# Optimization experiments

Hardware: AMD Instinct MI355X
Metric: run time of the kernel (lower is better)

Reference implementation:

```python
import jax, jax.numpy as jnp
import numpy as np

N = 100000
E = 1600000
IN_FEATS = 128
OUT_FEATS = 32


def setup_inputs() -> dict:
    key = jax.random.key(0)
    k1, k2, k3, k4, k5, k6 = jax.random.split(key, 6)
    features = jax.random.normal(k1, (N, IN_FEATS), dtype=jnp.float32)
    src = jax.random.randint(k2, (E,), 0, N, dtype=jnp.int32)
    dst = jax.random.randint(k3, (E,), 0, N, dtype=jnp.int32)
    # xavier_normal-like scale for fc_weight, attn vectors
    gain = float(np.sqrt(2.0))  # calculate_gain('relu')
    fc_std = gain * np.sqrt(2.0 / (IN_FEATS + OUT_FEATS))
    at_std = gain * np.sqrt(2.0 / (1 + OUT_FEATS))
    fc_weight = jax.random.normal(k4, (IN_FEATS, OUT_FEATS), dtype=jnp.float32) * fc_std
    attn_l = jax.random.normal(k5, (OUT_FEATS,), dtype=jnp.float32) * at_std
    attn_r = jax.random.normal(k6, (OUT_FEATS,), dtype=jnp.float32) * at_std
    return {"features": features, "src": src, "dst": dst,
            "fc_weight": fc_weight, "attn_l": attn_l, "attn_r": attn_r}


def reference(features, src, dst, fc_weight, attn_l, attn_r):
    # dense projection: [N, out]
    h = features @ fc_weight
    # per-node attention logits (GSDDMM operands)
    el = (h * attn_l).sum(-1)  # [N]
    er = (h * attn_r).sum(-1)  # [N]
    # SDDMM: edge score = el[u] + er[v], LeakyReLU(0.2)
    e = jax.nn.leaky_relu(el[src] + er[dst], negative_slope=0.2)  # [E]
    # edge softmax over destination node
    m = jax.ops.segment_max(e, dst, num_segments=N)  # [N], -inf for isolated nodes
    m = jnp.where(jnp.isfinite(m), m, 0.0)
    ex = jnp.exp(e - m[dst])
    s = jax.ops.segment_sum(ex, dst, num_segments=N)  # [N]
    alpha = ex / s[dst]  # [E]
    # SpMM: out[v] = sum_{(u,v) in E} h[u] * alpha[(u,v)]
    out = jax.ops.segment_sum(h[src] * alpha[:, None], dst, num_segments=N)  # [N, out]
    return out
```

## Files before the change

kernel.cpp:

```cpp
#include <hip/hip_runtime.h>
#include <math.h>

#define IN_FEATS 128
#define OUT_FEATS 32
#define BSHIFT 8
#define NPB 256
#define KMAX 512
#define CHUNK 4096
#define PEPT 8
#define CAPL 5120
#define RPT 5

__device__ __forceinline__ unsigned short f2bf(float f) {
    unsigned int u = __float_as_uint(f);
    u += 0x7FFFu + ((u >> 16) & 1u);
    return (unsigned short)(u >> 16);
}
__device__ __forceinline__ float bf2f_lo(unsigned int v) {
    return __uint_as_float(v << 16);
}
__device__ __forceinline__ float bf2f_hi(unsigned int v) {
    return __uint_as_float(v & 0xFFFF0000u);
}

__global__ __launch_bounds__(256) void proj_kernel(
    const float* __restrict__ features,
    const float* __restrict__ W,
    const float* __restrict__ attn_l,
    const float* __restrict__ attn_r,
    unsigned short* __restrict__ h,
    float* __restrict__ el,
    float* __restrict__ er,
    int N)
{
    __shared__ float Ws[IN_FEATS * OUT_FEATS];
    __shared__ float featT[4][IN_FEATS][16];

    const int t  = threadIdx.x;
    const int n0 = blockIdx.x * 64;

    {
        const float4* Wg = (const float4*)W;
        float4* Wl = (float4*)Ws;
#pragma unroll
        for (int i = 0; i < 4; ++i)
            Wl[t + 256 * i] = Wg[t + 256 * i];
    }

    {
        const int r = t >> 2;
        const int q = t & 3;
        const int wbuf = r >> 4;
        const int nl   = r & 15;
        if (n0 + r < N) {
            const float* frow = features + (size_t)(n0 + r) * IN_FEATS;
#pragma unroll
            for (int m = 0; m < 8; ++m) {
                int c = q * 8 + m;
                float4 f4 = *(const float4*)(frow + c * 4);
                featT[wbuf][c * 4 + 0][nl] = f4.x;
                featT[wbuf][c * 4 + 1][nl] = f4.y;
                featT[wbuf][c * 4 + 2][nl] = f4.z;
                featT[wbuf][c * 4 + 3][nl] = f4.w;
            }
        }
    }
    __syncthreads();

    const int wv   = t >> 6;
    const int lane = t & 63;
    const int jq   = lane & 7;
    const int ns   = lane >> 3;

    float4 acc0 = make_float4(0.f, 0.f, 0.f, 0.f);
    float4 acc1 = make_float4(0.f, 0.f, 0.f, 0.f);

#pragma unroll 16
    for (int k = 0; k < IN_FEATS; ++k) {
        float4 w4 = *(const float4*)&Ws[k * OUT_FEATS + jq * 4];
        float2 f2 = *(const float2*)&featT[wv][k][ns * 2];
        acc0.x += f2.x * w4.x; acc0.y += f2.x * w4.y;
        acc0.z += f2.x * w4.z; acc0.w += f2.x * w4.w;
        acc1.x += f2.y * w4.x; acc1.y += f2.y * w4.y;
        acc1.z += f2.y * w4.z; acc1.w += f2.y * w4.w;
    }

    const int node0 = n0 + wv * 16 + ns * 2;
    const float4 al4 = ((const float4*)attn_l)[jq];
    const float4 ar4 = ((const float4*)attn_r)[jq];

    float pl0 = acc0.x * al4.x + acc0.y * al4.y + acc0.z * al4.z + acc0.w * al4.w;
    float pr0 = acc0.x * ar4.x + acc0.y * ar4.y + acc0.z * ar4.z + acc0.w * ar4.w;
    float pl1 = acc1.x * al4.x + acc1.y * al4.y + acc1.z * al4.z + acc1.w * al4.w;
    float pr1 = acc1.x * ar4.x + acc1.y * ar4.y + acc1.z * ar4.z + acc1.w * ar4.w;
#pragma unroll
    for (int off = 1; off < 8; off <<= 1) {
        pl0 += __shfl_xor(pl0, off);
        pr0 += __shfl_xor(pr0, off);
        pl1 += __shfl_xor(pl1, off);
        pr1 += __shfl_xor(pr1, off);
    }

    if (node0 < N) {
        ushort4 p;
        p.x = f2bf(acc0.x); p.y = f2bf(acc0.y); p.z = f2bf(acc0.z); p.w = f2bf(acc0.w);
        *(ushort4*)(h + (size_t)node0 * OUT_FEATS + jq * 4) = p;
        if (jq == 0) { el[node0] = pl0; er[node0] = pr0; }
    }
    if (node0 + 1 < N) {
        ushort4 p;
        p.x = f2bf(acc1.x); p.y = f2bf(acc1.y); p.z = f2bf(acc1.z); p.w = f2bf(acc1.w);
        *(ushort4*)(h + (size_t)(node0 + 1) * OUT_FEATS + jq * 4) = p;
        if (jq == 0) { el[node0 + 1] = pl1; er[node0 + 1] = pr1; }
    }
}

__global__ __launch_bounds__(512) void init_cursor_kernel(
    int* __restrict__ gcursor, int K, int region)
{
    int b = blockIdx.x * blockDim.x + threadIdx.x;
    if (b < K) gcursor[b] = b * region;
}

__global__ __launch_bounds__(512) void partition_kernel(
    const int* __restrict__ src,
    const int* __restrict__ dst,
    int* __restrict__ gcursor,
    int* __restrict__ binned,
    int E, int region)
{
    __shared__ int hist[KMAX];
    __shared__ int lbase[KMAX];
    int t = threadIdx.x;
    if (t < KMAX) hist[t] = 0;
    __syncthreads();

    int base = blockIdx.x * CHUNK;
    int s_reg[PEPT], d_reg[PEPT], r_reg[PEPT];
#pragma unroll
    for (int i = 0; i < PEPT; ++i) {
        int idx = base + i * 512 + t;
        if (idx < E) {
            s_reg[i] = src[idx];
            d_reg[i] = dst[idx];
            r_reg[i] = atomicAdd(&hist[d_reg[i] >> BSHIFT], 1);
        } else d_reg[i] = -1;
    }
    __syncthreads();
    if (t < KMAX && hist[t] > 0) lbase[t] = atomicAdd(&gcursor[t], hist[t]);
    __syncthreads();
#pragma unroll
    for (int i = 0; i < PEPT; ++i) {
        if (d_reg[i] >= 0) {
            int b = d_reg[i] >> BSHIFT;
            int pos = lbase[b] + r_reg[i];
            if (pos < (b + 1) * region)
                binned[pos] = ((d_reg[i] & (NPB - 1)) << 17) | s_reg[i];
        }
    }
}

__global__ __launch_bounds__(1024) void bucket_agg_kernel(
    const int* __restrict__ binned,
    const int* __restrict__ gcursor,
    const unsigned short* __restrict__ h,
    const float* __restrict__ el,
    const float* __restrict__ er,
    float* __restrict__ out,
    int N, int region)
{
    __shared__ int lcnt[NPB];
    __shared__ int rowL[NPB];
    __shared__ int degL[NPB];
    __shared__ int wsum[4];
    __shared__ int slds[CAPL];

    const int b = blockIdx.x;
    const int t = threadIdx.x;
    const int estart = b * region;
    int bucketE = gcursor[b] - estart;
    bucketE = min(bucketE, min(region, CAPL));

    if (t < NPB) lcnt[t] = 0;
    __syncthreads();

    int recs[RPT], rnk[RPT];
#pragma unroll
    for (int c = 0; c < RPT; ++c) {
        int i = t + c * 1024;
        if (i < bucketE) {
            recs[c] = binned[estart + i];
            rnk[c]  = atomicAdd(&lcnt[recs[c] >> 17], 1);
        } else recs[c] = -1;
    }
    __syncthreads();

    if (t < NPB) {
        int v = lcnt[t];
        int x = v;
#pragma unroll
        for (int off = 1; off < 64; off <<= 1) {
            int y = __shfl_up(x, off);
            if ((t & 63) >= off) x += y;
        }
        if ((t & 63) == 63) wsum[t >> 6] = x;
        degL[t] = v;
        rowL[t] = x - v;
    }
    __syncthreads();
    if (t < NPB) {
        int wpre = 0;
#pragma unroll
        for (int ww = 0; ww < 4; ++ww)
            if (ww < (t >> 6)) wpre += wsum[ww];
        rowL[t] += wpre;
    }
    __syncthreads();

#pragma unroll
    for (int c = 0; c < RPT; ++c) {
        if (recs[c] >= 0)
            slds[rowL[recs[c] >> 17] + rnk[c]] = recs[c] & 0x1FFFF;
    }
    __syncthreads();

    const int w     = t >> 6;
    const int lane  = t & 63;
    const int half  = lane >> 5;
    const int l32   = lane & 31;
    const int quad  = l32 & 7;
    const int esub  = l32 >> 3;

    for (int nlp = w; nlp < NPB / 2; nlp += 16) {
        int nl   = nlp * 2 + half;
        int node = (b << BSHIFT) + nl;
        if (node >= N) continue;
        int d  = degL[nl];
        int rs = rowL[nl];

        float4 acc = make_float4(0.f, 0.f, 0.f, 0.f);
        float  s   = 0.f;
        float  er_n = (d > 0) ? er[node] : 0.f;

        for (int base = 0; base < d; base += 16) {
            int u[4];
#pragma unroll
            for (int r = 0; r < 4; ++r) {
                int i = base + esub + 4 * r;
                u[r] = (i < d) ? slds[rs + i] : -1;
            }
            float ee[4]; uint2 hh[4];
#pragma unroll
            for (int r = 0; r < 4; ++r) {
                if (u[r] >= 0) {
                    ee[r] = el[u[r]];
                    hh[r] = *(const uint2*)(h + (size_t)u[r] * OUT_FEATS + quad * 4);
                }
            }
#pragma unroll
            for (int r = 0; r < 4; ++r) {
                if (u[r] >= 0) {
                    float v = ee[r] + er_n;
                    v = (v > 0.f) ? v : 0.2f * v;
                    float a = __expf(v);
                    s += a;
                    acc.x += a * bf2f_lo(hh[r].x);
                    acc.y += a * bf2f_hi(hh[r].x);
                    acc.z += a * bf2f_lo(hh[r].y);
                    acc.w += a * bf2f_hi(hh[r].y);
                }
            }
        }
#pragma unroll
        for (int off = 8; off < 32; off <<= 1) {
            acc.x += __shfl_xor(acc.x, off);
            acc.y += __shfl_xor(acc.y, off);
            acc.z += __shfl_xor(acc.z, off);
            acc.w += __shfl_xor(acc.w, off);
            s     += __shfl_xor(s, off);
        }
        if (esub == 0) {
            float inv = (d > 0) ? 1.f / s : 0.f;
            float4 o = make_float4(acc.x * inv, acc.y * inv, acc.z * inv, acc.w * inv);
            *(float4*)(out + (size_t)node * OUT_FEATS + quad * 4) = o;
        }
    }
}

extern "C" void kernel_launch(void* const* d_in, const int* in_sizes, int n_in,
                              void* d_out, int out_size, void* d_ws, size_t ws_size,
                              hipStream_t stream)
{
    const float* features = (const float*)d_in[0];
    const int*   src      = (const int*)d_in[1];
    const int*   dst      = (const int*)d_in[2];
    const float* fc_w     = (const float*)d_in[3];
    const float* attn_l   = (const float*)d_in[4];
    const float* attn_r   = (const float*)d_in[5];

    const int N = in_sizes[0] / IN_FEATS;
    const int E = in_sizes[1];

    float* out = (float*)d_out;

    const int K = (N + NPB - 1) >> BSHIFT;
    const int reg = (E + K - 1) / K;
    int region = reg + 768;
    if (region > CAPL) region = CAPL;

    char* ws = (char*)d_ws;
    int*   binned  = (int*)ws;
    unsigned short* h = (unsigned short*)(binned + (size_t)K * region);
    float* el      = (float*)(h + (size_t)N * OUT_FEATS);
    float* er      = el + N;
    int*   gcursor = (int*)(er + N);

    proj_kernel<<<(N + 63) / 64, 256, 0, stream>>>(
        features, fc_w, attn_l, attn_r, h, el, er, N);

    init_cursor_kernel<<<(K + 511) / 512, 512, 0, stream>>>(gcursor, K, region);

    partition_kernel<<<(E + CHUNK - 1) / CHUNK, 512, 0, stream>>>(
        src, dst, gcursor, binned, E, region);

    bucket_agg_kernel<<<K, 1024, 0, stream>>>(
        binned, gcursor, h, el, er, out, N, region);
}
```

Measured before the change: 171.9 us.

## Fuse projection and edge partitioning into one launch with smaller node buckets

Merges the projection and edge-partition kernels into a single launch. Blocks below PB do the dense projection and the remaining blocks bin edges, sharing memory through a union, so the two independent stages run concurrently. The cursor-init kernel becomes a memset of per-bucket counts, and buckets shrink from 256 to 128 nodes, so twice as many aggregation blocks launch with 512 threads each. This cuts launch overhead and serial stage gaps, at the cost of more global atomics per partition block (1024 bins) and a tighter per-bucket capacity margin.

```diff
diff --git a/kernel.cpp b/kernel.cpp
--- a/kernel.cpp
+++ b/kernel.cpp
@@ -3,13 +3,13 @@
 
 #define IN_FEATS 128
 #define OUT_FEATS 32
-#define BSHIFT 8
-#define NPB 256
-#define KMAX 512
+#define BSHIFT 7
+#define NPB 128
+#define KMAX 1024
 #define CHUNK 4096
-#define PEPT 8
-#define CAPL 5120
-#define RPT 5
+#define PEPT 16
+#define CAPL 3072
+#define RPT 6
 
 __device__ __forceinline__ unsigned short f2bf(float f) {
     unsigned int u = __float_as_uint(f);
@@ -23,146 +23,140 @@
     return __uint_as_float(v & 0xFFFF0000u);
 }
 
-__global__ __launch_bounds__(256) void proj_kernel(
+union FusedSmem {
+    struct { float Ws[IN_FEATS * OUT_FEATS]; float featT[4][IN_FEATS][16]; } p;
+    struct { int hist[KMAX]; int lbase[KMAX]; } q;
+};
+
+__global__ __launch_bounds__(256) void proj_partition_kernel(
     const float* __restrict__ features,
     const float* __restrict__ W,
     const float* __restrict__ attn_l,
     const float* __restrict__ attn_r,
+    const int* __restrict__ src,
+    const int* __restrict__ dst,
     unsigned short* __restrict__ h,
     float* __restrict__ el,
     float* __restrict__ er,
-    int N)
+    int* __restrict__ gcount,
+    int* __restrict__ binned,
+    int N, int E, int PB, int region)
 {
-    __shared__ float Ws[IN_FEATS * OUT_FEATS];
-    __shared__ float featT[4][IN_FEATS][16];
-
-    const int t  = threadIdx.x;
-    const int n0 = blockIdx.x * 64;
-
-    {
-        const float4* Wg = (const float4*)W;
-        float4* Wl = (float4*)Ws;
-#pragma unroll
-        for (int i = 0; i < 4; ++i)
-            Wl[t + 256 * i] = Wg[t + 256 * i];
-    }
-
-    {
-        const int r = t >> 2;
-        const int q = t & 3;
-        const int wbuf = r >> 4;
-        const int nl   = r & 15;
-        if (n0 + r < N) {
-            const float* frow = features + (size_t)(n0 + r) * IN_FEATS;
-#pragma unroll
-            for (int m = 0; m < 8; ++m) {
-                int c = q * 8 + m;
-                float4 f4 = *(const float4*)(frow + c * 4);
-                featT[wbuf][c * 4 + 0][nl] = f4.x;
-                featT[wbuf][c * 4 + 1][nl] = f4.y;
-                featT[wbuf][c * 4 + 2][nl] = f4.z;
-                featT[wbuf][c * 4 + 3][nl] = f4.w;
-            }
-        }
-    }
-    __syncthreads();
-
-    const int wv   = t >> 6;
-    const int lane = t & 63;
-    const int jq   = lane & 7;
-    const int ns   = lane >> 3;
-
-    float4 acc0 = make_float4(0.f, 0.f, 0.f, 0.f);
-    float4 acc1 = make_float4(0.f, 0.f, 0.f, 0.f);
+    __shared__ FusedSmem sh;
+    const int t = threadIdx.x;
+
+    if ((int)blockIdx.x < PB) {
+        const int n0 = blockIdx.x * 64;
+
+        {
+            const float4* Wg = (const float4*)W;
+            float4* Wl = (float4*)sh.p.Ws;
+#pragma unroll
+            for (int i = 0; i < 4; ++i)
+                Wl[t + 256 * i] = Wg[t + 256 * i];
+        }
+        {
+            const int r = t >> 2;
+            const int q = t & 3;
+            const int wbuf = r >> 4;
+            const int nl   = r & 15;
+            if (n0 + r < N) {
+                const float* frow = features + (size_t)(n0 + r) * IN_FEATS;
+#pragma unroll
+                for (int m = 0; m < 8; ++m) {
+                    int c = q * 8 + m;
+                    float4 f4 = *(const float4*)(frow + c * 4);
+                    sh.p.featT[wbuf][c * 4 + 0][nl] = f4.x;
+                    sh.p.featT[wbuf][c * 4 + 1][nl] = f4.y;
+                    sh.p.featT[wbuf][c * 4 + 2][nl] = f4.z;
+                    sh.p.featT[wbuf][c * 4 + 3][nl] = f4.w;
+                }
+            }
+        }
+        __syncthreads();
+
+        const int wv   = t >> 6;
+        const int lane = t & 63;
+        const int jq   = lane & 7;
+        const int ns   = lane >> 3;
+
+        float4 acc0 = make_float4(0.f, 0.f, 0.f, 0.f);
+        float4 acc1 = make_float4(0.f, 0.f, 0.f, 0.f);
 
 #pragma unroll 16
-    for (int k = 0; k < IN_FEATS; ++k) {
-        float4 w4 = *(const float4*)&Ws[k * OUT_FEATS + jq * 4];
-        float2 f2 = *(const float2*)&featT[wv][k][ns * 2];
-        acc0.x += f2.x * w4.x; acc0.y += f2.x * w4.y;
-        acc0.z += f2.x * w4.z; acc0.w += f2.x * w4.w;
-        acc1.x += f2.y * w4.x; acc1.y += f2.y * w4.y;
-        acc1.z += f2.y * w4.z; acc1.w += f2.y * w4.w;
-    }
-
-    const int node0 = n0 + wv * 16 + ns * 2;
-    const float4 al4 = ((const float4*)attn_l)[jq];
-    const float4 ar4 = ((const float4*)attn_r)[jq];
-
-    float pl0 = acc0.x * al4.x + acc0.y * al4.y + acc0.z * al4.z + acc0.w * al4.w;
-    float pr0 = acc0.x * ar4.x + acc0.y * ar4.y + acc0.z * ar4.z + acc0.w * ar4.w;
-    float pl1 = acc1.x * al4.x + acc1.y * al4.y + acc1.z * al4.z + acc1.w * al4.w;
-    float pr1 = acc1.x * ar4.x + acc1.y * ar4.y + acc1.z * ar4.z + acc1.w * ar4.w;
-#pragma unroll
-    for (int off = 1; off < 8; off <<= 1) {
-        pl0 += __shfl_xor(pl0, off);
-        pr0 += __shfl_xor(pr0, off);
-        pl1 += __shfl_xor(pl1, off);
-        pr1 += __shfl_xor(pr1, off);
-    }
-
-    if (node0 < N) {
-        ushort4 p;
-        p.x = f2bf(acc0.x); p.y = f2bf(acc0.y); p.z = f2bf(acc0.z); p.w = f2bf(acc0.w);
-        *(ushort4*)(h + (size_t)node0 * OUT_FEATS + jq * 4) = p;
-        if (jq == 0) { el[node0] = pl0; er[node0] = pr0; }
-    }
-    if (node0 + 1 < N) {
-        ushort4 p;
-        p.x = f2bf(acc1.x); p.y = f2bf(acc1.y); p.z = f2bf(acc1.z); p.w = f2bf(acc1.w);
-        *(ushort4*)(h + (size_t)(node0 + 1) * OUT_FEATS + jq * 4) = p;
-        if (jq == 0) { el[node0 + 1] = pl1; er[node0 + 1] = pr1; }
-    }
-}
-
-__global__ __launch_bounds__(512) void init_cursor_kernel(
-    int* __restrict__ gcursor, int K, int region)
-{
-    int b = blockIdx.x * blockDim.x + threadIdx.x;
-    if (b < K) gcursor[b] = b * region;
-}
-
-__global__ __launch_bounds__(512) void partition_kernel(
-    const int* __restrict__ src,
-    const int* __restrict__ dst,
-    int* __restrict__ gcursor,
-    int* __restrict__ binned,
-    int E, int region)
-{
-    __shared__ int hist[KMAX];
-    __shared__ int lbase[KMAX];
-    int t = threadIdx.x;
-    if (t < KMAX) hist[t] = 0;
-    __syncthreads();
-
-    int base = blockIdx.x * CHUNK;
-    int s_reg[PEPT], d_reg[PEPT], r_reg[PEPT];
-#pragma unroll
-    for (int i = 0; i < PEPT; ++i) {
-        int idx = base + i * 512 + t;
-        if (idx < E) {
-            s_reg[i] = src[idx];
-            d_reg[i] = dst[idx];
-            r_reg[i] = atomicAdd(&hist[d_reg[i] >> BSHIFT], 1);
-        } else d_reg[i] = -1;
-    }
-    __syncthreads();
-    if (t < KMAX && hist[t] > 0) lbase[t] = atomicAdd(&gcursor[t], hist[t]);
-    __syncthreads();
-#pragma unroll
-    for (int i = 0; i < PEPT; ++i) {
-        if (d_reg[i] >= 0) {
-            int b = d_reg[i] >> BSHIFT;
-            int pos = lbase[b] + r_reg[i];
-            if (pos < (b + 1) * region)
-                binned[pos] = ((d_reg[i] & (NPB - 1)) << 17) | s_reg[i];
-        }
-    }
-}
-
-__global__ __launch_bounds__(1024) void bucket_agg_kernel(
+        for (int k = 0; k < IN_FEATS; ++k) {
+            float4 w4 = *(const float4*)&sh.p.Ws[k * OUT_FEATS + jq * 4];
+            float2 f2 = *(const float2*)&sh.p.featT[wv][k][ns * 2];
+            acc0.x += f2.x * w4.x; acc0.y += f2.x * w4.y;
+            acc0.z += f2.x * w4.z; acc0.w += f2.x * w4.w;
+            acc1.x += f2.y * w4.x; acc1.y += f2.y * w4.y;
+            acc1.z += f2.y * w4.z; acc1.w += f2.y * w4.w;
+        }
+
+        const int node0 = n0 + wv * 16 + ns * 2;
+        const float4 al4 = ((const float4*)attn_l)[jq];
+        const float4 ar4 = ((const float4*)attn_r)[jq];
+
+        float pl0 = acc0.x * al4.x + acc0.y * al4.y + acc0.z * al4.z + acc0.w * al4.w;
+        float pr0 = acc0.x * ar4.x + acc0.y * ar4.y + acc0.z * ar4.z + acc0.w * ar4.w;
+        float pl1 = acc1.x * al4.x + acc1.y * al4.y + acc1.z * al4.z + acc1.w * al4.w;
+        float pr1 = acc1.x * ar4.x + acc1.y * ar4.y + acc1.z * ar4.z + acc1.w * ar4.w;
+#pragma unroll
+        for (int off = 1; off < 8; off <<= 1) {
+            pl0 += __shfl_xor(pl0, off);
+            pr0 += __shfl_xor(pr0, off);
+            pl1 += __shfl_xor(pl1, off);
+            pr1 += __shfl_xor(pr1, off);
+        }
+
+        if (node0 < N) {
+            ushort4 p;
+            p.x = f2bf(acc0.x); p.y = f2bf(acc0.y); p.z = f2bf(acc0.z); p.w = f2bf(acc0.w);
+            *(ushort4*)(h + (size_t)node0 * OUT_FEATS + jq * 4) = p;
+            if (jq == 0) { el[node0] = pl0; er[node0] = pr0; }
+        }
+        if (node0 + 1 < N) {
+            ushort4 p;
+            p.x = f2bf(acc1.x); p.y = f2bf(acc1.y); p.z = f2bf(acc1.z); p.w = f2bf(acc1.w);
+            *(ushort4*)(h + (size_t)(node0 + 1) * OUT_FEATS + jq * 4) = p;
+            if (jq == 0) { el[node0 + 1] = pl1; er[node0 + 1] = pr1; }
+        }
+    } else {
+        for (int i = t; i < KMAX; i += 256) sh.q.hist[i] = 0;
+        __syncthreads();
+
+        int base = (blockIdx.x - PB) * CHUNK;
+        int s_reg[PEPT], d_reg[PEPT], r_reg[PEPT];
+#pragma unroll
+        for (int i = 0; i < PEPT; ++i) {
+            int idx = base + i * 256 + t;
+            if (idx < E) {
+                s_reg[i] = src[idx];
+                d_reg[i] = dst[idx];
+                r_reg[i] = atomicAdd(&sh.q.hist[d_reg[i] >> BSHIFT], 1);
+            } else d_reg[i] = -1;
+        }
+        __syncthreads();
+        for (int bb = t; bb < KMAX; bb += 256)
+            if (sh.q.hist[bb] > 0)
+                sh.q.lbase[bb] = atomicAdd(&gcount[bb], sh.q.hist[bb]);
+        __syncthreads();
+#pragma unroll
+        for (int i = 0; i < PEPT; ++i) {
+            if (d_reg[i] >= 0) {
+                int bb = d_reg[i] >> BSHIFT;
+                int off = sh.q.lbase[bb] + r_reg[i];
+                if (off < region)
+                    binned[(size_t)bb * region + off] =
+                        ((d_reg[i] & (NPB - 1)) << 17) | s_reg[i];
+            }
+        }
+    }
+}
+
+__global__ __launch_bounds__(512) void bucket_agg_kernel(
     const int* __restrict__ binned,
-    const int* __restrict__ gcursor,
+    const int* __restrict__ gcount,
     const unsigned short* __restrict__ h,
     const float* __restrict__ el,
     const float* __restrict__ er,
@@ -172,14 +166,13 @@
     __shared__ int lcnt[NPB];
     __shared__ int rowL[NPB];
     __shared__ int degL[NPB];
-    __shared__ int wsum[4];
+    __shared__ int wsum[2];
     __shared__ int slds[CAPL];
 
     const int b = blockIdx.x;
     const int t = threadIdx.x;
-    const int estart = b * region;
-    int bucketE = gcursor[b] - estart;
-    bucketE = min(bucketE, min(region, CAPL));
+    const size_t estart = (size_t)b * region;
+    int bucketE = min(gcount[b], region);
 
     if (t < NPB) lcnt[t] = 0;
     __syncthreads();
@@ -187,7 +180,7 @@
     int recs[RPT], rnk[RPT];
 #pragma unroll
     for (int c = 0; c < RPT; ++c) {
-        int i = t + c * 1024;
+        int i = t + c * 512;
         if (i < bucketE) {
             recs[c] = binned[estart + i];
             rnk[c]  = atomicAdd(&lcnt[recs[c] >> 17], 1);
@@ -208,13 +201,7 @@
         rowL[t] = x - v;
     }
     __syncthreads();
-    if (t < NPB) {
-        int wpre = 0;
-#pragma unroll
-        for (int ww = 0; ww < 4; ++ww)
-            if (ww < (t >> 6)) wpre += wsum[ww];
-        rowL[t] += wpre;
-    }
+    if (t < NPB && (t >> 6) == 1) rowL[t] += wsum[0];
     __syncthreads();
 
 #pragma unroll
@@ -231,7 +218,7 @@
     const int quad  = l32 & 7;
     const int esub  = l32 >> 3;
 
-    for (int nlp = w; nlp < NPB / 2; nlp += 16) {
+    for (int nlp = w; nlp < NPB / 2; nlp += 8) {
         int nl   = nlp * 2 + half;
         int node = (b << BSHIFT) + nl;
         if (node >= N) continue;
@@ -305,24 +292,25 @@
 
     const int K = (N + NPB - 1) >> BSHIFT;
     const int reg = (E + K - 1) / K;
-    int region = reg + 768;
+    int region = reg + 512;
     if (region > CAPL) region = CAPL;
+
+    const int PB = (N + 63) / 64;
+    const int QB = (E + CHUNK - 1) / CHUNK;
 
     char* ws = (char*)d_ws;
     int*   binned  = (int*)ws;
     unsigned short* h = (unsigned short*)(binned + (size_t)K * region);
     float* el      = (float*)(h + (size_t)N * OUT_FEATS);
     float* er      = el + N;
-    int*   gcursor = (int*)(er + N);
-
-    proj_kernel<<<(N + 63) / 64, 256, 0, stream>>>(
-        features, fc_w, attn_l, attn_r, h, el, er, N);
-
-    init_cursor_kernel<<<(K + 511) / 512, 512, 0, stream>>>(gcursor, K, region);
-
-    partition_kernel<<<(E + CHUNK - 1) / CHUNK, 512, 0, stream>>>(
-        src, dst, gcursor, binned, E, region);
-
-    bucket_agg_kernel<<<K, 1024, 0, stream>>>(
-        binned, gcursor, h, el, er, out, N, region);
-}
+    int*   gcount  = (int*)(er + N);
+
+    hipMemsetAsync(gcount, 0, (size_t)K * sizeof(int), stream);
+
+    proj_partition_kernel<<<PB + QB, 256, 0, stream>>>(
+        features, fc_w, attn_l, attn_r, src, dst,
+        h, el, er, gcount, binned, N, E, PB, region);
+
+    bucket_agg_kernel<<<K, 512, 0, stream>>>(
+        binned, gcount, h, el, er, out, N, region);
+}
```

Measured after the change: 173.6 us. Within noise of the previous version (+1.0%).
